# Kernel optimization log

Measured on AMD Instinct MI355X. Metric: run time of the kernel, lower is better.

Reference implementation:

```python
import jax, jax.numpy as jnp
import numpy as np

R, A14, X, N0, N1, NH = 8192, 14, 3, 256, 256, 8
A = R * A14


def _sqrt(x):
    return (jnp.abs(x) + 1e-06) ** 0.5 * (x >= 0.0).astype(x.dtype)


def _mlp(x, layers):
    # layers: list of (w, b_or_None); leaky_relu between layers, not after last
    n = len(layers)
    for i, (w, b) in enumerate(layers):
        x = x @ w
        if b is not None:
            x = x + b
        if i < n - 1:
            x = jax.nn.leaky_relu(x)
    return x


def _lin_init(key, fan_in, fan_out):
    return jax.random.normal(key, (fan_in, fan_out), dtype=jnp.float32) / np.sqrt(fan_in)


def setup_inputs() -> dict:
    key = jax.random.key(0)
    ks = jax.random.split(key, 16)
    q = jax.random.normal(ks[0], (A, N0), dtype=jnp.float32)
    p = jax.random.normal(ks[1], (A, X, N0), dtype=jnp.float32)
    atom_mask = jax.random.randint(ks[2], (R, A14), 0, 2).astype(jnp.float32)
    # sam MLP: (N0 + N0) -> N0 -> N0 -> 2*NH
    sam_w1 = _lin_init(ks[3], 2 * N0, N0); sam_b1 = jnp.zeros((N0,), jnp.float32)
    sam_w2 = _lin_init(ks[4], N0, N0);      sam_b2 = jnp.zeros((N0,), jnp.float32)
    sam_w3 = _lin_init(ks[5], N0, 2 * NH);  sam_b3 = jnp.zeros((2 * NH,), jnp.float32)
    # zdm MLP: N0*NH -> N0 -> N0 -> N1
    zdm_w1 = _lin_init(ks[6], N0 * NH, N0); zdm_b1 = jnp.zeros((N0,), jnp.float32)
    zdm_w2 = _lin_init(ks[7], N0, N0);       zdm_b2 = jnp.zeros((N0,), jnp.float32)
    zdm_w3 = _lin_init(ks[8], N0, N1);       zdm_b3 = jnp.zeros((N1,), jnp.float32)
    # zdm_vec: N0*NH -> N1, no bias
    zdm_vec_w = _lin_init(ks[9], N0 * NH, N1)
    return dict(q=q, p=p, atom_mask=atom_mask,
                sam_w1=sam_w1, sam_b1=sam_b1, sam_w2=sam_w2, sam_b2=sam_b2,
                sam_w3=sam_w3, sam_b3=sam_b3,
                zdm_w1=zdm_w1, zdm_b1=zdm_b1, zdm_w2=zdm_w2, zdm_b2=zdm_b2,
                zdm_w3=zdm_w3, zdm_b3=zdm_b3, zdm_vec_w=zdm_vec_w)


def reference(q, p, atom_mask,
              sam_w1, sam_b1, sam_w2, sam_b2, sam_w3, sam_b3,
              zdm_w1, zdm_b1, zdm_w2, zdm_b2, zdm_w3, zdm_b3, zdm_vec_w):
    r, a14 = atom_mask.shape
    # norm(p, axis=1): sqrt of sum of squares over the vector (X) axis -> [A, C]
    z = jnp.concatenate([q, _sqrt((p * p).sum(axis=1))], axis=1)  # [A, 2*N0]
    sam_out = _mlp(z, [(sam_w1, sam_b1), (sam_w2, sam_b2), (sam_w3, sam_b3)])  # [A, 2*NH]
    sa = sam_out.reshape(r, a14, 2 * NH)
    q_ = q.reshape(r, a14, N0)
    p_ = p.reshape(r, a14, X, N0)
    # masked softmax over atoms within each residue
    logit_mask = (1.0 - atom_mask + 1e-06) / (atom_mask - 1e-06)  # [r, a14]
    aw = jax.nn.softmax(sa + logit_mask[:, :, None], axis=1)       # [r, a14, 2*NH]
    aw = aw.reshape(r, a14, NH, 2)
    qh = jnp.einsum('rac,rah->rch', q_, aw[..., 0])                # [r, N0, NH]
    ph = jnp.einsum('raxc,rah->rxch', p_, aw[..., 1])              # [r, X, N0, NH]
    qh_flat = qh.reshape(r, -1)          # [r, N0*NH]
    ph_flat = ph.reshape(r, X, -1)       # [r, X, N0*NH]
    res_mask = jnp.any(atom_mask.astype(bool), axis=-1).astype(ph_flat.dtype)
    qh_flat = qh_flat * res_mask[:, None]
    ph_flat = ph_flat * res_mask[:, None, None]
    qr = _mlp(qh_flat, [(zdm_w1, zdm_b1), (zdm_w2, zdm_b2), (zdm_w3, zdm_b3)])  # [r, N1]
    pr = ph_flat @ zdm_vec_w                                                     # [r, X, N1]
    return (qr, pr)
```

## Files before the change

### kernel.cpp

```cpp
#include <hip/hip_runtime.h>
#include <hip/hip_bf16.h>

#define R_TOT   8192
#define A14     14
#define A_TOT   (R_TOT * A14)
#define QR_ELEMS (R_TOT * 256)

typedef __attribute__((ext_vector_type(8))) short bf16x8;
typedef __attribute__((ext_vector_type(4))) float f32x4;
typedef __attribute__((ext_vector_type(4))) short short4v;

#define MFMA16(a, b, c) __builtin_amdgcn_mfma_f32_16x16x32_bf16((a), (b), (c), 0, 0, 0)

static __device__ __forceinline__ float b2f(short s) {
    return __uint_as_float(((unsigned)(unsigned short)s) << 16);
}

__global__ __launch_bounds__(256) void wtrans_kernel(
    const float* __restrict__ w, __hip_bfloat16* __restrict__ wT, int K, int N)
{
    __shared__ float tile[32][33];
    const int kb = blockIdx.x * 32, nb = blockIdx.y * 32;
    const int tx = threadIdx.x & 31, ty = threadIdx.x >> 5;
    #pragma unroll
    for (int i = 0; i < 32; i += 8) {
        int k = kb + ty + i, n = nb + tx;
        tile[ty + i][tx] = (k < K && n < N) ? w[(size_t)k * N + n] : 0.f;
    }
    __syncthreads();
    #pragma unroll
    for (int i = 0; i < 32; i += 8) {
        int n = nb + ty + i, k = kb + tx;
        if (n < N && k < K) wT[(size_t)n * K + k] = __float2bfloat16(tile[tx][ty + i]);
    }
}

__global__ __launch_bounds__(256, 2) void sampool_kernel(
    const float* __restrict__ q, const float* __restrict__ p,
    const float* __restrict__ atom_mask,
    const __hip_bfloat16* __restrict__ wT1, const float* __restrict__ b1,
    const __hip_bfloat16* __restrict__ wT2, const float* __restrict__ b2,
    const __hip_bfloat16* __restrict__ wT3, const float* __restrict__ b3,
    __hip_bfloat16* __restrict__ qh, __hip_bfloat16* __restrict__ ph)
{
    __shared__ __align__(16) __hip_bfloat16 zl[64][520];
    __shared__ float sa_lds[64][16];
    __shared__ float aw_lds[2][4][14][8];

    const int tid = threadIdx.x;
    const int r0  = blockIdx.x * 4;
    const int a0  = r0 * A14;
    const int wv  = tid >> 6;
    const int l   = tid & 63;
    const int lr  = l & 15;
    const int lh  = l >> 4;
    const int nbase = wv * 64;

    #pragma unroll 4
    for (int it = 0; it < 32; ++it) {
        const int g  = tid + it * 256;
        const int m  = g >> 7;
        const int c4 = (g & 127) * 4;
        const int ar = a0 + m;
        const size_t arow = (size_t)((ar < A_TOT) ? ar : (A_TOT - 1));
        __hip_bfloat16 t[4];
        if (c4 < 256) {
            const float4 v = *(const float4*)&q[arow * 256 + c4];
            t[0] = __float2bfloat16(v.x); t[1] = __float2bfloat16(v.y);
            t[2] = __float2bfloat16(v.z); t[3] = __float2bfloat16(v.w);
        } else {
            const int cc = c4 - 256;
            const float4 pa = *(const float4*)&p[arow * 768 + 0 * 256 + cc];
            const float4 pb = *(const float4*)&p[arow * 768 + 1 * 256 + cc];
            const float4 pc = *(const float4*)&p[arow * 768 + 2 * 256 + cc];
            t[0] = __float2bfloat16(sqrtf(pa.x*pa.x + pb.x*pb.x + pc.x*pc.x + 1e-6f));
            t[1] = __float2bfloat16(sqrtf(pa.y*pa.y + pb.y*pb.y + pc.y*pc.y + 1e-6f));
            t[2] = __float2bfloat16(sqrtf(pa.z*pa.z + pb.z*pb.z + pc.z*pc.z + 1e-6f));
            t[3] = __float2bfloat16(sqrtf(pa.w*pa.w + pb.w*pb.w + pc.w*pc.w + 1e-6f));
        }
        *(short4v*)&zl[m][c4] = *(const short4v*)t;
    }
    __syncthreads();

    {
        f32x4 acc[4][4] = {};
        const __hip_bfloat16* pB[4];
        #pragma unroll
        for (int nt = 0; nt < 4; ++nt)
            pB[nt] = wT1 + (size_t)(nbase + nt * 16 + lr) * 512 + lh * 8;
        bf16x8 bc[4], b1v[4];
        #pragma unroll
        for (int nt = 0; nt < 4; ++nt) { bc[nt]  = *(const bf16x8*)(pB[nt]);
                                         b1v[nt] = *(const bf16x8*)(pB[nt] + 32); }
        bf16x8 ac[4];
        #pragma unroll
        for (int mf = 0; mf < 4; ++mf)
            ac[mf] = *(const bf16x8*)&zl[mf * 16 + lr][lh * 8];

        #pragma unroll
        for (int k0 = 0; k0 < 512; k0 += 32) {
            bf16x8 b2v[4], an[4];
            if (k0 + 64 < 512) {
                #pragma unroll
                for (int nt = 0; nt < 4; ++nt)
                    b2v[nt] = *(const bf16x8*)(pB[nt] + k0 + 64);
            }
            if (k0 + 32 < 512) {
                #pragma unroll
                for (int mf = 0; mf < 4; ++mf)
                    an[mf] = *(const bf16x8*)&zl[mf * 16 + lr][k0 + 32 + lh * 8];
            }
            #pragma unroll
            for (int mf = 0; mf < 4; ++mf)
                #pragma unroll
                for (int nt = 0; nt < 4; ++nt)
                    acc[mf][nt] = MFMA16(ac[mf], bc[nt], acc[mf][nt]);
            #pragma unroll
            for (int nt = 0; nt < 4; ++nt) { bc[nt] = b1v[nt]; b1v[nt] = b2v[nt]; }
            #pragma unroll
            for (int mf = 0; mf < 4; ++mf) ac[mf] = an[mf];
        }
        __syncthreads();
        #pragma unroll
        for (int nt = 0; nt < 4; ++nt) {
            const int n = nbase + nt * 16 + lr;
            const float bv = b1[n];
            #pragma unroll
            for (int mf = 0; mf < 4; ++mf)
                #pragma unroll
                for (int v = 0; v < 4; ++v) {
                    float x = acc[mf][nt][v] + bv;
                    x = x >= 0.f ? x : 0.01f * x;
                    zl[mf * 16 + lh * 4 + v][256 + n] = __float2bfloat16(x);
                }
        }
    }
    __syncthreads();

    {
        f32x4 acc[4][4] = {};
        const __hip_bfloat16* pB[4];
        #pragma unroll
        for (int nt = 0; nt < 4; ++nt)
            pB[nt] = wT2 + (size_t)(nbase + nt * 16 + lr) * 256 + lh * 8;
        bf16x8 bc[4], b1v[4];
        #pragma unroll
        for (int nt = 0; nt < 4; ++nt) { bc[nt]  = *(const bf16x8*)(pB[nt]);
                                         b1v[nt] = *(const bf16x8*)(pB[nt] + 32); }
        bf16x8 ac[4];
        #pragma unroll
        for (int mf = 0; mf < 4; ++mf)
            ac[mf] = *(const bf16x8*)&zl[mf * 16 + lr][256 + lh * 8];

        #pragma unroll
        for (int k0 = 0; k0 < 256; k0 += 32) {
            bf16x8 b2v[4], an[4];
            if (k0 + 64 < 256) {
                #pragma unroll
                for (int nt = 0; nt < 4; ++nt)
                    b2v[nt] = *(const bf16x8*)(pB[nt] + k0 + 64);
            }
            if (k0 + 32 < 256) {
                #pragma unroll
                for (int mf = 0; mf < 4; ++mf)
                    an[mf] = *(const bf16x8*)&zl[mf * 16 + lr][256 + k0 + 32 + lh * 8];
            }
            #pragma unroll
            for (int mf = 0; mf < 4; ++mf)
                #pragma unroll
                for (int nt = 0; nt < 4; ++nt)
                    acc[mf][nt] = MFMA16(ac[mf], bc[nt], acc[mf][nt]);
            #pragma unroll
            for (int nt = 0; nt < 4; ++nt) { bc[nt] = b1v[nt]; b1v[nt] = b2v[nt]; }
            #pragma unroll
            for (int mf = 0; mf < 4; ++mf) ac[mf] = an[mf];
        }
        __syncthreads();
        #pragma unroll
        for (int nt = 0; nt < 4; ++nt) {
            const int n = nbase + nt * 16 + lr;
            const float bv = b2[n];
            #pragma unroll
            for (int mf = 0; mf < 4; ++mf)
                #pragma unroll
                for (int v = 0; v < 4; ++v) {
                    float x = acc[mf][nt][v] + bv;
                    x = x >= 0.f ? x : 0.01f * x;
                    zl[mf * 16 + lh * 4 + v][256 + n] = __float2bfloat16(x);
                }
        }
    }
    __syncthreads();

    {
        f32x4 a3 = {};
        const __hip_bfloat16* pW3 = wT3 + (size_t)lr * 256 + lh * 8;
        bf16x8 bwc = *(const bf16x8*)(pW3);
        bf16x8 bw1 = *(const bf16x8*)(pW3 + 32);
        #pragma unroll
        for (int k0 = 0; k0 < 256; k0 += 32) {
            bf16x8 bw2;
            if (k0 + 64 < 256) bw2 = *(const bf16x8*)(pW3 + k0 + 64);
            const bf16x8 af = *(const bf16x8*)&zl[wv * 16 + lr][256 + k0 + lh * 8];
            a3 = MFMA16(af, bwc, a3);
            bwc = bw1; bw1 = bw2;
        }
        const float bv = b3[lr];
        #pragma unroll
        for (int v = 0; v < 4; ++v)
            sa_lds[wv * 16 + lh * 4 + v][lr] = a3[v] + bv;
    }
    __syncthreads();

    if (tid < 64) {
        const int res = tid >> 4, ch = tid & 15;
        const size_t rg = (size_t)(r0 + res);
        float sl[14];
        float mx = -3.0e38f, anym = 0.f;
        #pragma unroll
        for (int a = 0; a < 14; ++a) {
            const float m = atom_mask[rg * 14 + a];
            anym = fmaxf(anym, m);
            const float lm = (1.0f - m + 1e-6f) / (m - 1e-6f);
            const float v = sa_lds[res * 14 + a][ch] + lm;
            sl[a] = v;
            mx = fmaxf(mx, v);
        }
        float s = 0.f;
        #pragma unroll
        for (int a = 0; a < 14; ++a) { sl[a] = expf(sl[a] - mx); s += sl[a]; }
        const float inv = ((anym != 0.f) ? 1.f : 0.f) / s;
        const int h = ch >> 1;
        #pragma unroll
        for (int a = 0; a < 14; ++a)
            aw_lds[ch & 1][res][a][h] = sl[a] * inv;
    }
    __syncthreads();

    #pragma unroll
    for (int jr = 0; jr < 4; ++jr) {
        const int job = tid + jr * 256;
        const int res = job >> 8;
        const int s   = (job >> 6) & 3;
        const int c4  = (job & 63) * 4;
        const size_t rg = (size_t)(r0 + res);
        const float* const aw = &aw_lds[(s == 0) ? 0 : 1][res][0][0];
        float acc4[4][8] = {};
        if (s == 0) {
            #pragma unroll
            for (int a = 0; a < 14; ++a) {
                const short4v qv = *(const short4v*)&zl[res * 14 + a][c4];
                const float qf[4] = { b2f(qv.x), b2f(qv.y), b2f(qv.z), b2f(qv.w) };
                #pragma unroll
                for (int ci = 0; ci < 4; ++ci)
                    #pragma unroll
                    for (int h = 0; h < 8; ++h)
                        acc4[ci][h] = fmaf(qf[ci], aw[a * 8 + h], acc4[ci][h]);
            }
        } else {
            const int x = s - 1;
            #pragma unroll
            for (int a = 0; a < 14; ++a) {
                const float4 pv = *(const float4*)&p[(rg * 14 + a) * 768 + (size_t)x * 256 + c4];
                const float pf[4] = { pv.x, pv.y, pv.z, pv.w };
                #pragma unroll
                for (int ci = 0; ci < 4; ++ci)
                    #pragma unroll
                    for (int h = 0; h < 8; ++h)
                        acc4[ci][h] = fmaf(pf[ci], aw[a * 8 + h], acc4[ci][h]);
            }
        }
        alignas(16) __hip_bfloat16 tmp[32];
        #pragma unroll
        for (int ci = 0; ci < 4; ++ci)
            #pragma unroll
            for (int h = 0; h < 8; ++h)
                tmp[ci * 8 + h] = __float2bfloat16(acc4[ci][h]);
        __hip_bfloat16* const dst = (s == 0)
            ? &qh[rg * 2048 + (size_t)c4 * 8]
            : &ph[(rg * 3 + (s - 1)) * 2048 + (size_t)c4 * 8];
        #pragma unroll
        for (int u = 0; u < 4; ++u)
            *reinterpret_cast<int4*>(dst + u * 8) = *reinterpret_cast<const int4*>(tmp + u * 8);
    }
}

__global__ __launch_bounds__(256, 3) void zdm_kernel(
    const __hip_bfloat16* __restrict__ x, const __hip_bfloat16* __restrict__ zT1,
    const float* __restrict__ zb1, const __hip_bfloat16* __restrict__ zT2,
    const float* __restrict__ zb2, const __hip_bfloat16* __restrict__ zT3,
    const float* __restrict__ zb3, float* __restrict__ qr)
{
    __shared__ __align__(16) __hip_bfloat16 xl[2][32][264];
    __shared__ __align__(16) __hip_bfloat16 hl[32][264];

    const int tid = threadIdx.x;
    const int a0  = blockIdx.x * 32;
    const int wv  = tid >> 6;
    const int l   = tid & 63;
    const int lr  = l & 15;
    const int lh  = l >> 4;
    const int nbase = wv * 64;

    int4 st[4];
    #define LOADC(c)                                                          \
        { _Pragma("unroll")                                                   \
          for (int it = 0; it < 4; ++it) {                                    \
              const int g = tid + it * 256;                                   \
              const int m = g >> 5, c8 = (g & 31) * 8;                        \
              st[it] = *(const int4*)&x[(size_t)(a0 + m) * 2048 + (c) * 256 + c8]; } }
    #define WRITEC(buf)                                                       \
        { _Pragma("unroll")                                                   \
          for (int it = 0; it < 4; ++it) {                                    \
              const int g = tid + it * 256;                                   \
              const int m = g >> 5, c8 = (g & 31) * 8;                        \
              *(int4*)&xl[buf][m][c8] = st[it]; } }

    f32x4 acc[2][4] = {};
    {
        const __hip_bfloat16* pB[4];
        #pragma unroll
        for (int nt = 0; nt < 4; ++nt)
            pB[nt] = zT1 + (size_t)(nbase + nt * 16 + lr) * 2048 + lh * 8;

        LOADC(0); WRITEC(0); __syncthreads();
        for (int c = 0; c < 8; ++c) {
            if (c < 7) LOADC(c + 1);
            const __hip_bfloat16 (* const cur)[264] = xl[c & 1];
            bf16x8 bc[4];
            #pragma unroll
            for (int nt = 0; nt < 4; ++nt) bc[nt] = *(const bf16x8*)(pB[nt] + c * 256);
            #pragma unroll
            for (int k0 = 0; k0 < 256; k0 += 32) {
                bf16x8 bn[4];
                if (k0 + 32 < 256) {
                    #pragma unroll
                    for (int nt = 0; nt < 4; ++nt)
                        bn[nt] = *(const bf16x8*)(pB[nt] + c * 256 + k0 + 32);
                }
                const int kc = k0 + lh * 8;
                const bf16x8 a0f = *(const bf16x8*)&cur[lr][kc];
                const bf16x8 a1f = *(const bf16x8*)&cur[16 + lr][kc];
                #pragma unroll
                for (int nt = 0; nt < 4; ++nt) {
                    acc[0][nt] = MFMA16(a0f, bc[nt], acc[0][nt]);
                    acc[1][nt] = MFMA16(a1f, bc[nt], acc[1][nt]);
                }
                #pragma unroll
                for (int nt = 0; nt < 4; ++nt) bc[nt] = bn[nt];
            }
            if (c < 7) WRITEC((c + 1) & 1);
            __syncthreads();
        }
        #pragma unroll
        for (int nt = 0; nt < 4; ++nt) {
            const int n = nbase + nt * 16 + lr;
            const float bv = zb1[n];
            #pragma unroll
            for (int mt = 0; mt < 2; ++mt)
                #pragma unroll
                for (int v = 0; v < 4; ++v) {
                    float xv = acc[mt][nt][v] + bv;
                    xv = xv >= 0.f ? xv : 0.01f * xv;
                    hl[mt * 16 + lh * 4 + v][n] = __float2bfloat16(xv);
                }
        }
    }
    __syncthreads();

    {
        f32x4 acc2[2][4] = {};
        const __hip_bfloat16* pB[4];
        #pragma unroll
        for (int nt = 0; nt < 4; ++nt)
            pB[nt] = zT2 + (size_t)(nbase + nt * 16 + lr) * 256 + lh * 8;
        bf16x8 bc[4];
        #pragma unroll
        for (int nt = 0; nt < 4; ++nt) bc[nt] = *(const bf16x8*)(pB[nt]);
        #pragma unroll
        for (int k0 = 0; k0 < 256; k0 += 32) {
            bf16x8 bn[4];
            if (k0 + 32 < 256) {
                #pragma unroll
                for (int nt = 0; nt < 4; ++nt)
                    bn[nt] = *(const bf16x8*)(pB[nt] + k0 + 32);
            }
            const int kc = k0 + lh * 8;
            const bf16x8 a0f = *(const bf16x8*)&hl[lr][kc];
            const bf16x8 a1f = *(const bf16x8*)&hl[16 + lr][kc];
            #pragma unroll
            for (int nt = 0; nt < 4; ++nt) {
                acc2[0][nt] = MFMA16(a0f, bc[nt], acc2[0][nt]);
                acc2[1][nt] = MFMA16(a1f, bc[nt], acc2[1][nt]);
            }
            #pragma unroll
            for (int nt = 0; nt < 4; ++nt) bc[nt] = bn[nt];
        }
        __syncthreads();
        #pragma unroll
        for (int nt = 0; nt < 4; ++nt) {
            const int n = nbase + nt * 16 + lr;
            const float bv = zb2[n];
            #pragma unroll
            for (int mt = 0; mt < 2; ++mt)
                #pragma unroll
                for (int v = 0; v < 4; ++v) {
                    float xv = acc2[mt][nt][v] + bv;
                    xv = xv >= 0.f ? xv : 0.01f * xv;
                    hl[mt * 16 + lh * 4 + v][n] = __float2bfloat16(xv);
                }
        }
    }
    __syncthreads();

    {
        f32x4 acc3[2][4] = {};
        const __hip_bfloat16* pB[4];
        #pragma unroll
        for (int nt = 0; nt < 4; ++nt)
            pB[nt] = zT3 + (size_t)(nbase + nt * 16 + lr) * 256 + lh * 8;
        bf16x8 bc[4];
        #pragma unroll
        for (int nt = 0; nt < 4; ++nt) bc[nt] = *(const bf16x8*)(pB[nt]);
        #pragma unroll
        for (int k0 = 0; k0 < 256; k0 += 32) {
            bf16x8 bn[4];
            if (k0 + 32 < 256) {
                #pragma unroll
                for (int nt = 0; nt < 4; ++nt)
                    bn[nt] = *(const bf16x8*)(pB[nt] + k0 + 32);
            }
            const int kc = k0 + lh * 8;
            const bf16x8 a0f = *(const bf16x8*)&hl[lr][kc];
            const bf16x8 a1f = *(const bf16x8*)&hl[16 + lr][kc];
            #pragma unroll
            for (int nt = 0; nt < 4; ++nt) {
                acc3[0][nt] = MFMA16(a0f, bc[nt], acc3[0][nt]);
                acc3[1][nt] = MFMA16(a1f, bc[nt], acc3[1][nt]);
            }
            #pragma unroll
            for (int nt = 0; nt < 4; ++nt) bc[nt] = bn[nt];
        }
        #pragma unroll
        for (int nt = 0; nt < 4; ++nt) {
            const int n = nbase + nt * 16 + lr;
            const float bv = zb3[n];
            #pragma unroll
            for (int mt = 0; mt < 2; ++mt)
                #pragma unroll
                for (int v = 0; v < 4; ++v)
                    qr[(size_t)(a0 + mt * 16 + lh * 4 + v) * 256 + n] = acc3[mt][nt][v] + bv;
        }
    }
    #undef LOADC
    #undef WRITEC
}

__global__ __launch_bounds__(256, 3) void pr_kernel(
    const __hip_bfloat16* __restrict__ x, const __hip_bfloat16* __restrict__ vT,
    float* __restrict__ out)
{
    __shared__ __align__(16) __hip_bfloat16 xl[2][32][264];

    const int tid = threadIdx.x;
    const int a0  = blockIdx.x * 32;
    const int wv  = tid >> 6;
    const int l   = tid & 63;
    const int lr  = l & 15;
    const int lh  = l >> 4;
    const int nbase = wv * 64;

    int4 st[4];
    #define LOADC(c)                                                          \
        { _Pragma("unroll")                                                   \
          for (int it = 0; it < 4; ++it) {                                    \
              const int g = tid + it * 256;                                   \
              const int m = g >> 5, c8 = (g & 31) * 8;                        \
              st[it] = *(const int4*)&x[(size_t)(a0 + m) * 2048 + (c) * 256 + c8]; } }
    #define WRITEC(buf)                                                       \
        { _Pragma("unroll")                                                   \
          for (int it = 0; it < 4; ++it) {                                    \
              const int g = tid + it * 256;                                   \
              const int m = g >> 5, c8 = (g & 31) * 8;                        \
              *(int4*)&xl[buf][m][c8] = st[it]; } }

    f32x4 acc[2][4] = {};
    const __hip_bfloat16* pB[4];
    #pragma unroll
    for (int nt = 0; nt < 4; ++nt)
        pB[nt] = vT + (size_t)(nbase + nt * 16 + lr) * 2048 + lh * 8;

    LOADC(0); WRITEC(0); __syncthreads();
    for (int c = 0; c < 8; ++c) {
        if (c < 7) LOADC(c + 1);
        const __hip_bfloat16 (* const cur)[264] = xl[c & 1];
        bf16x8 bc[4];
        #pragma unroll
        for (int nt = 0; nt < 4; ++nt) bc[nt] = *(const bf16x8*)(pB[nt] + c * 256);
        #pragma unroll
        for (int k0 = 0; k0 < 256; k0 += 32) {
            bf16x8 bn[4];
            if (k0 + 32 < 256) {
                #pragma unroll
                for (int nt = 0; nt < 4; ++nt)
                    bn[nt] = *(const bf16x8*)(pB[nt] + c * 256 + k0 + 32);
            }
            const int kc = k0 + lh * 8;
            const bf16x8 a0f = *(const bf16x8*)&cur[lr][kc];
            const bf16x8 a1f = *(const bf16x8*)&cur[16 + lr][kc];
            #pragma unroll
            for (int nt = 0; nt < 4; ++nt) {
                acc[0][nt] = MFMA16(a0f, bc[nt], acc[0][nt]);
                acc[1][nt] = MFMA16(a1f, bc[nt], acc[1][nt]);
            }
            #pragma unroll
            for (int nt = 0; nt < 4; ++nt) bc[nt] = bn[nt];
        }
        if (c < 7) WRITEC((c + 1) & 1);
        __syncthreads();
    }
    #pragma unroll
    for (int nt = 0; nt < 4; ++nt) {
        const int n = nbase + nt * 16 + lr;
        #pragma unroll
        for (int mt = 0; mt < 2; ++mt)
            #pragma unroll
            for (int v = 0; v < 4; ++v)
                out[(size_t)(a0 + mt * 16 + lh * 4 + v) * 256 + n] = acc[mt][nt][v];
    }
    #undef LOADC
    #undef WRITEC
}

extern "C" void kernel_launch(void* const* d_in, const int* in_sizes, int n_in,
                              void* d_out, int out_size, void* d_ws, size_t ws_size,
                              hipStream_t stream)
{
    const float* q    = (const float*)d_in[0];
    const float* p    = (const float*)d_in[1];
    const float* amsk = (const float*)d_in[2];
    const float* sw1  = (const float*)d_in[3];
    const float* sb1  = (const float*)d_in[4];
    const float* sw2  = (const float*)d_in[5];
    const float* sb2  = (const float*)d_in[6];
    const float* sw3  = (const float*)d_in[7];
    const float* sb3  = (const float*)d_in[8];
    const float* zw1  = (const float*)d_in[9];
    const float* zb1  = (const float*)d_in[10];
    const float* zw2  = (const float*)d_in[11];
    const float* zb2  = (const float*)d_in[12];
    const float* zw3  = (const float*)d_in[13];
    const float* zb3  = (const float*)d_in[14];
    const float* zvw  = (const float*)d_in[15];

    char* ws = (char*)d_ws;
    size_t off = 0;
    __hip_bfloat16* qh   = (__hip_bfloat16*)(ws + off);  off += (size_t)R_TOT * 2048 * 2;
    __hip_bfloat16* ph   = (__hip_bfloat16*)(ws + off);  off += (size_t)R_TOT * 3 * 2048 * 2;
    __hip_bfloat16* wT1  = (__hip_bfloat16*)(ws + off);  off += 256 * 512 * 2;
    __hip_bfloat16* wT2  = (__hip_bfloat16*)(ws + off);  off += 256 * 256 * 2;
    __hip_bfloat16* wT3  = (__hip_bfloat16*)(ws + off);  off += 16 * 256 * 2;
    __hip_bfloat16* zT1  = (__hip_bfloat16*)(ws + off);  off += 256 * 2048 * 2;
    __hip_bfloat16* zT2  = (__hip_bfloat16*)(ws + off);  off += 256 * 256 * 2;
    __hip_bfloat16* zT3  = (__hip_bfloat16*)(ws + off);  off += 256 * 256 * 2;
    __hip_bfloat16* vT   = (__hip_bfloat16*)(ws + off);  off += 256 * 2048 * 2;

    float* qr = (float*)d_out;
    float* pr = (float*)d_out + QR_ELEMS;

    wtrans_kernel<<<dim3(16, 8), 256, 0, stream>>>(sw1, wT1, 512, 256);
    wtrans_kernel<<<dim3(8, 8),  256, 0, stream>>>(sw2, wT2, 256, 256);
    wtrans_kernel<<<dim3(8, 1),  256, 0, stream>>>(sw3, wT3, 256, 16);
    wtrans_kernel<<<dim3(64, 8), 256, 0, stream>>>(zw1, zT1, 2048, 256);
    wtrans_kernel<<<dim3(8, 8),  256, 0, stream>>>(zw2, zT2, 256, 256);
    wtrans_kernel<<<dim3(8, 8),  256, 0, stream>>>(zw3, zT3, 256, 256);
    wtrans_kernel<<<dim3(64, 8), 256, 0, stream>>>(zvw, vT, 2048, 256);

    sampool_kernel<<<R_TOT / 4, 256, 0, stream>>>(q, p, amsk, wT1, sb1, wT2, sb2, wT3, sb3, qh, ph);
    zdm_kernel<<<R_TOT / 32, 256, 0, stream>>>(qh, zT1, zb1, zT2, zb2, zT3, zb3, qr);
    pr_kernel<<<(R_TOT * 3) / 32, 256, 0, stream>>>(ph, vT, pr);

    (void)in_sizes; (void)n_in; (void)out_size; (void)ws_size;
}
```

Before: 496.6 us.

## Merge weight-transpose and tail launches; split sampool M across eight waves

The seven weight-transpose launches become one kernel that selects its matrix and tile from a flat block index. The zdm and pr kernels are merged into one launch whose first 256 blocks run the zdm MLP and whose remaining blocks run the vector projection. sampool now uses 512 threads, splitting the 64 atom rows between two groups of waves so each wave holds half the accumulators. This cuts launch count and gaps between kernels and raises waves per block, at the cost of idle waves in the small third layer.

```diff
diff --git a/kernel.cpp b/kernel.cpp
--- a/kernel.cpp
+++ b/kernel.cpp
@@ -16,26 +16,51 @@
     return __uint_as_float(((unsigned)(unsigned short)s) << 16);
 }
 
-__global__ __launch_bounds__(256) void wtrans_kernel(
-    const float* __restrict__ w, __hip_bfloat16* __restrict__ wT, int K, int N)
+static __device__ __forceinline__ void wtrans_tile(
+    const float* __restrict__ w, __hip_bfloat16* __restrict__ wT,
+    int K, int N, int kb, int nb, float* tile )
 {
-    __shared__ float tile[32][33];
-    const int kb = blockIdx.x * 32, nb = blockIdx.y * 32;
     const int tx = threadIdx.x & 31, ty = threadIdx.x >> 5;
     #pragma unroll
     for (int i = 0; i < 32; i += 8) {
         int k = kb + ty + i, n = nb + tx;
-        tile[ty + i][tx] = (k < K && n < N) ? w[(size_t)k * N + n] : 0.f;
+        tile[(ty + i) * 33 + tx] = (k < K && n < N) ? w[(size_t)k * N + n] : 0.f;
     }
     __syncthreads();
     #pragma unroll
     for (int i = 0; i < 32; i += 8) {
         int n = nb + ty + i, k = kb + tx;
-        if (n < N && k < K) wT[(size_t)n * K + k] = __float2bfloat16(tile[tx][ty + i]);
+        if (n < N && k < K) wT[(size_t)n * K + k] = __float2bfloat16(tile[tx * 33 + ty + i]);
     }
 }
 
-__global__ __launch_bounds__(256, 2) void sampool_kernel(
+__global__ __launch_bounds__(256) void wtrans_all_kernel(
+    const float* __restrict__ sw1, __hip_bfloat16* __restrict__ wT1,
+    const float* __restrict__ sw2, __hip_bfloat16* __restrict__ wT2,
+    const float* __restrict__ sw3, __hip_bfloat16* __restrict__ wT3,
+    const float* __restrict__ zw1, __hip_bfloat16* __restrict__ zT1,
+    const float* __restrict__ zw2, __hip_bfloat16* __restrict__ zT2,
+    const float* __restrict__ zw3, __hip_bfloat16* __restrict__ zT3,
+    const float* __restrict__ zvw, __hip_bfloat16* __restrict__ vT)
+{
+    __shared__ float tile[32 * 33];
+    int b = blockIdx.x;
+    if (b < 128)      { wtrans_tile(sw1, wT1, 512, 256, (b % 16) * 32, (b / 16) * 32, tile); return; }
+    b -= 128;
+    if (b < 64)       { wtrans_tile(sw2, wT2, 256, 256, (b % 8) * 32, (b / 8) * 32, tile); return; }
+    b -= 64;
+    if (b < 8)        { wtrans_tile(sw3, wT3, 256, 16,  b * 32, 0, tile); return; }
+    b -= 8;
+    if (b < 512)      { wtrans_tile(zw1, zT1, 2048, 256, (b % 64) * 32, (b / 64) * 32, tile); return; }
+    b -= 512;
+    if (b < 64)       { wtrans_tile(zw2, zT2, 256, 256, (b % 8) * 32, (b / 8) * 32, tile); return; }
+    b -= 64;
+    if (b < 64)       { wtrans_tile(zw3, zT3, 256, 256, (b % 8) * 32, (b / 8) * 32, tile); return; }
+    b -= 64;
+    wtrans_tile(zvw, vT, 2048, 256, (b % 64) * 32, (b / 64) * 32, tile);
+}
+
+__global__ __launch_bounds__(512, 2) void sampool_kernel(
     const float* __restrict__ q, const float* __restrict__ p,
     const float* __restrict__ atom_mask,
     const __hip_bfloat16* __restrict__ wT1, const float* __restrict__ b1,
@@ -54,11 +79,12 @@
     const int l   = tid & 63;
     const int lr  = l & 15;
     const int lh  = l >> 4;
-    const int nbase = wv * 64;
+    const int mbase = (wv >> 2) * 32;
+    const int nbase = (wv & 3) * 64;
 
     #pragma unroll 4
-    for (int it = 0; it < 32; ++it) {
-        const int g  = tid + it * 256;
+    for (int it = 0; it < 16; ++it) {
+        const int g  = tid + it * 512;
         const int m  = g >> 7;
         const int c4 = (g & 127) * 4;
         const int ar = a0 + m;
@@ -83,7 +109,7 @@
     __syncthreads();
 
     {
-        f32x4 acc[4][4] = {};
+        f32x4 acc[2][4] = {};
         const __hip_bfloat16* pB[4];
         #pragma unroll
         for (int nt = 0; nt < 4; ++nt)
@@ -92,14 +118,14 @@
         #pragma unroll
         for (int nt = 0; nt < 4; ++nt) { bc[nt]  = *(const bf16x8*)(pB[nt]);
                                          b1v[nt] = *(const bf16x8*)(pB[nt] + 32); }
-        bf16x8 ac[4];
-        #pragma unroll
-        for (int mf = 0; mf < 4; ++mf)
-            ac[mf] = *(const bf16x8*)&zl[mf * 16 + lr][lh * 8];
+        bf16x8 ac[2];
+        #pragma unroll
+        for (int mf = 0; mf < 2; ++mf)
+            ac[mf] = *(const bf16x8*)&zl[mbase + mf * 16 + lr][lh * 8];
 
         #pragma unroll
         for (int k0 = 0; k0 < 512; k0 += 32) {
-            bf16x8 b2v[4], an[4];
+            bf16x8 b2v[4], an[2];
             if (k0 + 64 < 512) {
                 #pragma unroll
                 for (int nt = 0; nt < 4; ++nt)
@@ -107,18 +133,18 @@
             }
             if (k0 + 32 < 512) {
                 #pragma unroll
-                for (int mf = 0; mf < 4; ++mf)
-                    an[mf] = *(const bf16x8*)&zl[mf * 16 + lr][k0 + 32 + lh * 8];
-            }
-            #pragma unroll
-            for (int mf = 0; mf < 4; ++mf)
+                for (int mf = 0; mf < 2; ++mf)
+                    an[mf] = *(const bf16x8*)&zl[mbase + mf * 16 + lr][k0 + 32 + lh * 8];
+            }
+            #pragma unroll
+            for (int mf = 0; mf < 2; ++mf)
                 #pragma unroll
                 for (int nt = 0; nt < 4; ++nt)
                     acc[mf][nt] = MFMA16(ac[mf], bc[nt], acc[mf][nt]);
             #pragma unroll
             for (int nt = 0; nt < 4; ++nt) { bc[nt] = b1v[nt]; b1v[nt] = b2v[nt]; }
             #pragma unroll
-            for (int mf = 0; mf < 4; ++mf) ac[mf] = an[mf];
+            for (int mf = 0; mf < 2; ++mf) ac[mf] = an[mf];
         }
         __syncthreads();
         #pragma unroll
@@ -126,19 +152,19 @@
             const int n = nbase + nt * 16 + lr;
             const float bv = b1[n];
             #pragma unroll
-            for (int mf = 0; mf < 4; ++mf)
+            for (int mf = 0; mf < 2; ++mf)
                 #pragma unroll
                 for (int v = 0; v < 4; ++v) {
                     float x = acc[mf][nt][v] + bv;
                     x = x >= 0.f ? x : 0.01f * x;
-                    zl[mf * 16 + lh * 4 + v][256 + n] = __float2bfloat16(x);
+                    zl[mbase + mf * 16 + lh * 4 + v][256 + n] = __float2bfloat16(x);
                 }
         }
     }
     __syncthreads();
 
     {
-        f32x4 acc[4][4] = {};
+        f32x4 acc[2][4] = {};
         const __hip_bfloat16* pB[4];
         #pragma unroll
         for (int nt = 0; nt < 4; ++nt)
@@ -147,14 +173,14 @@
         #pragma unroll
         for (int nt = 0; nt < 4; ++nt) { bc[nt]  = *(const bf16x8*)(pB[nt]);
                                          b1v[nt] = *(const bf16x8*)(pB[nt] + 32); }
-        bf16x8 ac[4];
-        #pragma unroll
-        for (int mf = 0; mf < 4; ++mf)
-            ac[mf] = *(const bf16x8*)&zl[mf * 16 + lr][256 + lh * 8];
+        bf16x8 ac[2];
+        #pragma unroll
+        for (int mf = 0; mf < 2; ++mf)
+            ac[mf] = *(const bf16x8*)&zl[mbase + mf * 16 + lr][256 + lh * 8];
 
         #pragma unroll
         for (int k0 = 0; k0 < 256; k0 += 32) {
-            bf16x8 b2v[4], an[4];
+            bf16x8 b2v[4], an[2];
             if (k0 + 64 < 256) {
                 #pragma unroll
                 for (int nt = 0; nt < 4; ++nt)
@@ -162,18 +188,18 @@
             }
             if (k0 + 32 < 256) {
                 #pragma unroll
-                for (int mf = 0; mf < 4; ++mf)
-                    an[mf] = *(const bf16x8*)&zl[mf * 16 + lr][256 + k0 + 32 + lh * 8];
-            }
-            #pragma unroll
-            for (int mf = 0; mf < 4; ++mf)
+                for (int mf = 0; mf < 2; ++mf)
+                    an[mf] = *(const bf16x8*)&zl[mbase + mf * 16 + lr][256 + k0 + 32 + lh * 8];
+            }
+            #pragma unroll
+            for (int mf = 0; mf < 2; ++mf)
                 #pragma unroll
                 for (int nt = 0; nt < 4; ++nt)
                     acc[mf][nt] = MFMA16(ac[mf], bc[nt], acc[mf][nt]);
             #pragma unroll
             for (int nt = 0; nt < 4; ++nt) { bc[nt] = b1v[nt]; b1v[nt] = b2v[nt]; }
             #pragma unroll
-            for (int mf = 0; mf < 4; ++mf) ac[mf] = an[mf];
+            for (int mf = 0; mf < 2; ++mf) ac[mf] = an[mf];
         }
         __syncthreads();
         #pragma unroll
@@ -181,18 +207,18 @@
             const int n = nbase + nt * 16 + lr;
             const float bv = b2[n];
             #pragma unroll
-            for (int mf = 0; mf < 4; ++mf)
+            for (int mf = 0; mf < 2; ++mf)
                 #pragma unroll
                 for (int v = 0; v < 4; ++v) {
                     float x = acc[mf][nt][v] + bv;
                     x = x >= 0.f ? x : 0.01f * x;
-                    zl[mf * 16 + lh * 4 + v][256 + n] = __float2bfloat16(x);
+                    zl[mbase + mf * 16 + lh * 4 + v][256 + n] = __float2bfloat16(x);
                 }
         }
     }
     __syncthreads();
 
-    {
+    if (wv < 4) {
         f32x4 a3 = {};
         const __hip_bfloat16* pW3 = wT3 + (size_t)lr * 256 + lh * 8;
         bf16x8 bwc = *(const bf16x8*)(pW3);
@@ -238,8 +264,8 @@
     __syncthreads();
 
     #pragma unroll
-    for (int jr = 0; jr < 4; ++jr) {
-        const int job = tid + jr * 256;
+    for (int jr = 0; jr < 2; ++jr) {
+        const int job = tid + jr * 512;
         const int res = job >> 8;
         const int s   = (job >> 6) & 3;
         const int c4  = (job & 63) * 4;
@@ -285,22 +311,27 @@
     }
 }
 
-__global__ __launch_bounds__(256, 3) void zdm_kernel(
-    const __hip_bfloat16* __restrict__ x, const __hip_bfloat16* __restrict__ zT1,
-    const float* __restrict__ zb1, const __hip_bfloat16* __restrict__ zT2,
-    const float* __restrict__ zb2, const __hip_bfloat16* __restrict__ zT3,
-    const float* __restrict__ zb3, float* __restrict__ qr)
+__global__ __launch_bounds__(256, 3) void tail_kernel(
+    const __hip_bfloat16* __restrict__ qh, const __hip_bfloat16* __restrict__ ph,
+    const __hip_bfloat16* __restrict__ zT1, const float* __restrict__ zb1,
+    const __hip_bfloat16* __restrict__ zT2, const float* __restrict__ zb2,
+    const __hip_bfloat16* __restrict__ zT3, const float* __restrict__ zb3,
+    const __hip_bfloat16* __restrict__ vT,
+    float* __restrict__ qr, float* __restrict__ pr)
 {
     __shared__ __align__(16) __hip_bfloat16 xl[2][32][264];
     __shared__ __align__(16) __hip_bfloat16 hl[32][264];
 
     const int tid = threadIdx.x;
-    const int a0  = blockIdx.x * 32;
     const int wv  = tid >> 6;
     const int l   = tid & 63;
     const int lr  = l & 15;
     const int lh  = l >> 4;
     const int nbase = wv * 64;
+    const bool is_zdm = (blockIdx.x < 256);
+    const int a0 = (is_zdm ? blockIdx.x : (blockIdx.x - 256)) * 32;
+    const __hip_bfloat16* const x = is_zdm ? qh : ph;
+    const __hip_bfloat16* const w1 = is_zdm ? zT1 : vT;
 
     int4 st[4];
     #define LOADC(c)                                                          \
@@ -321,7 +352,7 @@
         const __hip_bfloat16* pB[4];
         #pragma unroll
         for (int nt = 0; nt < 4; ++nt)
-            pB[nt] = zT1 + (size_t)(nbase + nt * 16 + lr) * 2048 + lh * 8;
+            pB[nt] = w1 + (size_t)(nbase + nt * 16 + lr) * 2048 + lh * 8;
 
         LOADC(0); WRITEC(0); __syncthreads();
         for (int c = 0; c < 8; ++c) {
@@ -352,19 +383,33 @@
             if (c < 7) WRITEC((c + 1) & 1);
             __syncthreads();
         }
+    }
+
+    if (!is_zdm) {
         #pragma unroll
         for (int nt = 0; nt < 4; ++nt) {
             const int n = nbase + nt * 16 + lr;
-            const float bv = zb1[n];
             #pragma unroll
             for (int mt = 0; mt < 2; ++mt)
                 #pragma unroll
-                for (int v = 0; v < 4; ++v) {
-                    float xv = acc[mt][nt][v] + bv;
-                    xv = xv >= 0.f ? xv : 0.01f * xv;
-                    hl[mt * 16 + lh * 4 + v][n] = __float2bfloat16(xv);
-                }
-        }
+                for (int v = 0; v < 4; ++v)
+                    pr[(size_t)(a0 + mt * 16 + lh * 4 + v) * 256 + n] = acc[mt][nt][v];
+        }
+        return;
+    }
+
+    #pragma unroll
+    for (int nt = 0; nt < 4; ++nt) {
+        const int n = nbase + nt * 16 + lr;
+        const float bv = zb1[n];
+        #pragma unroll
+        for (int mt = 0; mt < 2; ++mt)
+            #pragma unroll
+            for (int v = 0; v < 4; ++v) {
+                float xv = acc[mt][nt][v] + bv;
+                xv = xv >= 0.f ? xv : 0.01f * xv;
+                hl[mt * 16 + lh * 4 + v][n] = __float2bfloat16(xv);
+            }
     }
     __syncthreads();
 
@@ -451,82 +496,6 @@
                 for (int v = 0; v < 4; ++v)
                     qr[(size_t)(a0 + mt * 16 + lh * 4 + v) * 256 + n] = acc3[mt][nt][v] + bv;
         }
-    }
-    #undef LOADC
-    #undef WRITEC
-}
-
-__global__ __launch_bounds__(256, 3) void pr_kernel(
-    const __hip_bfloat16* __restrict__ x, const __hip_bfloat16* __restrict__ vT,
-    float* __restrict__ out)
-{
-    __shared__ __align__(16) __hip_bfloat16 xl[2][32][264];
-
-    const int tid = threadIdx.x;
-    const int a0  = blockIdx.x * 32;
-    const int wv  = tid >> 6;
-    const int l   = tid & 63;
-    const int lr  = l & 15;
-    const int lh  = l >> 4;
-    const int nbase = wv * 64;
-
-    int4 st[4];
-    #define LOADC(c)                                                          \
-        { _Pragma("unroll")                                                   \
-          for (int it = 0; it < 4; ++it) {                                    \
-              const int g = tid + it * 256;                                   \
-              const int m = g >> 5, c8 = (g & 31) * 8;                        \
-              st[it] = *(const int4*)&x[(size_t)(a0 + m) * 2048 + (c) * 256 + c8]; } }
-    #define WRITEC(buf)                                                       \
-        { _Pragma("unroll")                                                   \
-          for (int it = 0; it < 4; ++it) {                                    \
-              const int g = tid + it * 256;                                   \
-              const int m = g >> 5, c8 = (g & 31) * 8;                        \
-              *(int4*)&xl[buf][m][c8] = st[it]; } }
-
-    f32x4 acc[2][4] = {};
-    const __hip_bfloat16* pB[4];
-    #pragma unroll
-    for (int nt = 0; nt < 4; ++nt)
-        pB[nt] = vT + (size_t)(nbase + nt * 16 + lr) * 2048 + lh * 8;
-
-    LOADC(0); WRITEC(0); __syncthreads();
-    for (int c = 0; c < 8; ++c) {
-        if (c < 7) LOADC(c + 1);
-        const __hip_bfloat16 (* const cur)[264] = xl[c & 1];
-        bf16x8 bc[4];
-        #pragma unroll
-        for (int nt = 0; nt < 4; ++nt) bc[nt] = *(const bf16x8*)(pB[nt] + c * 256);
-        #pragma unroll
-        for (int k0 = 0; k0 < 256; k0 += 32) {
-            bf16x8 bn[4];
-            if (k0 + 32 < 256) {
-                #pragma unroll
-                for (int nt = 0; nt < 4; ++nt)
-                    bn[nt] = *(const bf16x8*)(pB[nt] + c * 256 + k0 + 32);
-            }
-            const int kc = k0 + lh * 8;
-            const bf16x8 a0f = *(const bf16x8*)&cur[lr][kc];
-            const bf16x8 a1f = *(const bf16x8*)&cur[16 + lr][kc];
-            #pragma unroll
-            for (int nt = 0; nt < 4; ++nt) {
-                acc[0][nt] = MFMA16(a0f, bc[nt], acc[0][nt]);
-                acc[1][nt] = MFMA16(a1f, bc[nt], acc[1][nt]);
-            }
-            #pragma unroll
-            for (int nt = 0; nt < 4; ++nt) bc[nt] = bn[nt];
-        }
-        if (c < 7) WRITEC((c + 1) & 1);
-        __syncthreads();
-    }
-    #pragma unroll
-    for (int nt = 0; nt < 4; ++nt) {
-        const int n = nbase + nt * 16 + lr;
-        #pragma unroll
-        for (int mt = 0; mt < 2; ++mt)
-            #pragma unroll
-            for (int v = 0; v < 4; ++v)
-                out[(size_t)(a0 + mt * 16 + lh * 4 + v) * 256 + n] = acc[mt][nt][v];
     }
     #undef LOADC
     #undef WRITEC
@@ -568,17 +537,10 @@
     float* qr = (float*)d_out;
     float* pr = (float*)d_out + QR_ELEMS;
 
-    wtrans_kernel<<<dim3(16, 8), 256, 0, stream>>>(sw1, wT1, 512, 256);
-    wtrans_kernel<<<dim3(8, 8),  256, 0, stream>>>(sw2, wT2, 256, 256);
-    wtrans_kernel<<<dim3(8, 1),  256, 0, stream>>>(sw3, wT3, 256, 16);
-    wtrans_kernel<<<dim3(64, 8), 256, 0, stream>>>(zw1, zT1, 2048, 256);
-    wtrans_kernel<<<dim3(8, 8),  256, 0, stream>>>(zw2, zT2, 256, 256);
-    wtrans_kernel<<<dim3(8, 8),  256, 0, stream>>>(zw3, zT3, 256, 256);
-    wtrans_kernel<<<dim3(64, 8), 256, 0, stream>>>(zvw, vT, 2048, 256);
-
-    sampool_kernel<<<R_TOT / 4, 256, 0, stream>>>(q, p, amsk, wT1, sb1, wT2, sb2, wT3, sb3, qh, ph);
-    zdm_kernel<<<R_TOT / 32, 256, 0, stream>>>(qh, zT1, zb1, zT2, zb2, zT3, zb3, qr);
-    pr_kernel<<<(R_TOT * 3) / 32, 256, 0, stream>>>(ph, vT, pr);
+    wtrans_all_kernel<<<1352, 256, 0, stream>>>(sw1, wT1, sw2, wT2, sw3, wT3,
+                                                zw1, zT1, zw2, zT2, zw3, zT3, zvw, vT);
+    sampool_kernel<<<R_TOT / 4, 512, 0, stream>>>(q, p, amsk, wT1, sb1, wT2, sb2, wT3, sb3, qh, ph);
+    tail_kernel<<<1024, 256, 0, stream>>>(qh, ph, zT1, zb1, zT2, zb2, zT3, zb3, vT, qr, pr);
 
     (void)in_sizes; (void)n_in; (void)out_size; (void)ws_size;
 }
```

Measured after the change: 558.7 us. 12.5% more time.
